# Kernel tuning notes

Measured on AMD Instinct MI355X. Metric: run time of the kernel, lower is better.

The kernel has to match this reference:

```python
import jax, jax.numpy as jnp
import numpy as np

INPUT_DIM = 1024
HIDDEN_DIM = 1024

def setup_inputs() -> dict:
    key = jax.random.key(0)
    ks = jax.random.split(key, 9)
    s_in = 1.0 / np.sqrt(INPUT_DIM)
    s_h = 1.0 / np.sqrt(HIDDEN_DIM)
    x = jax.random.normal(ks[0], (4, 2048, INPUT_DIM), dtype=jnp.float32)
    Wq = jax.random.uniform(ks[1], (INPUT_DIM, HIDDEN_DIM), jnp.float32, -s_in, s_in)
    bq = jax.random.uniform(ks[2], (HIDDEN_DIM,), jnp.float32, -s_in, s_in)
    Wk = jax.random.uniform(ks[3], (INPUT_DIM, HIDDEN_DIM), jnp.float32, -s_in, s_in)
    bk = jax.random.uniform(ks[4], (HIDDEN_DIM,), jnp.float32, -s_in, s_in)
    Wv = jax.random.uniform(ks[5], (INPUT_DIM, HIDDEN_DIM), jnp.float32, -s_in, s_in)
    bv = jax.random.uniform(ks[6], (HIDDEN_DIM,), jnp.float32, -s_in, s_in)
    Wo = jax.random.uniform(ks[7], (HIDDEN_DIM, INPUT_DIM), jnp.float32, -s_h, s_h)
    bo = jax.random.uniform(ks[8], (INPUT_DIM,), jnp.float32, -s_h, s_h)
    return {"x": x, "Wq": Wq, "bq": bq, "Wk": Wk, "bk": bk, "Wv": Wv, "bv": bv, "Wo": Wo, "bo": bo}

def reference(x, Wq, bq, Wk, bk, Wv, bv, Wo, bo):
    # x: [B, S, D_in]; scale uses x.shape[-1] (faithful to source, which divides by sqrt(input_dim))
    scale = 1.0 / jnp.sqrt(jnp.asarray(x.shape[-1], dtype=x.dtype))
    Q = jnp.einsum('bsd,dh->bsh', x, Wq) + bq
    K = jnp.einsum('bsd,dh->bsh', x, Wk) + bk
    V = jnp.einsum('bsd,dh->bsh', x, Wv) + bv
    scores = jnp.einsum('bqh,bkh->bqk', Q, K) * scale  # [B, S, S]
    attn = jax.nn.softmax(scores, axis=-1)
    ctx = jnp.einsum('bqk,bkh->bqh', attn, V)
    return jnp.einsum('bsh,hd->bsd', ctx, Wo) + bo
```

## Files before the change

### kernel.cpp

```cpp
#include <hip/hip_runtime.h>
#include <hip/hip_bf16.h>

typedef __attribute__((ext_vector_type(8))) short bf16x8;
typedef __attribute__((ext_vector_type(16))) float f32x16;
typedef __attribute__((ext_vector_type(4))) unsigned short us4;

#define AS1 __attribute__((address_space(1)))
#define AS3 __attribute__((address_space(3)))

__device__ __forceinline__ unsigned short f2bf(float f) {
  unsigned u = __float_as_uint(f);
  u += 0x7fff + ((u >> 16) & 1);
  return (unsigned short)(u >> 16);
}

__device__ __forceinline__ float bf2f(unsigned short h) {
  return __uint_as_float((unsigned)h << 16);
}

__device__ __forceinline__ void gload_lds16(const void* g, void* l) {
  __builtin_amdgcn_global_load_lds((const AS1 unsigned int*)g,
                                   (AS3 unsigned int*)l, 16, 0, 0);
}

template <typename OutT, bool BIAS, int MODE, int NJ>
__global__ __launch_bounds__(256, (NJ >= 3) ? 2 : 3) void gemm_bt(
    const unsigned short* __restrict__ A,
    const unsigned short* __restrict__ Bt,
    OutT* __restrict__ C,
    unsigned short* __restrict__ Vt,
    const float* __restrict__ bias,
    int Kd, int lda, int ldb, int ldc,
    long sA, long sB, long sC,
    float scale) {
  constexpr int BN    = NJ * 64;
  constexpr int ROWS  = 128 + BN;
  constexpr int SLOTS = ROWS / 16;
  __shared__ unsigned short lds[2][ROWS * 32];

  const int bz = blockIdx.z;
  A  += (size_t)bz * sA + (size_t)blockIdx.x * 128 * lda;
  Bt += (size_t)bz * sB + (size_t)blockIdx.y * BN * ldb;

  const int tid  = threadIdx.x;
  const int wave = tid >> 6;
  const int lane = tid & 63;
  const int wm   = (wave >> 1) * 64;
  const int wn   = (wave & 1) * (NJ * 32);
  const int l32  = lane & 31;
  const int half = lane >> 5;
  const int cg   = ((lane & 3) ^ ((lane >> 2) & 3) ^ (lane >> 4)) * 8;
  const int pswz = (l32 & 3) ^ ((l32 >> 2) & 3);

  auto stage = [&](int k0, int b) {
#pragma unroll
    for (int j = 0; j < SLOTS / 4; ++j) {
      const int s = wave + 4 * j;
      const int r = s * 16 + (lane >> 2);
      const unsigned short* src = (s < 8) ? (A + (size_t)r * lda)
                                          : (Bt + (size_t)(r - 128) * ldb);
      gload_lds16(src + k0 + cg, (char*)&lds[b][0] + s * 1024);
    }
  };

  f32x16 acc[2][NJ] = {};

  stage(0, 0);
  int cur = 0;
  for (int k0 = 0; k0 < Kd; k0 += 32) {
    __syncthreads();
    if (k0 + 32 < Kd) stage(k0 + 32, cur ^ 1);

    const unsigned short* base = &lds[cur][0];
    bf16x8 af[2][2], bfr[NJ][2];
#pragma unroll
    for (int t = 0; t < 2; ++t)
#pragma unroll
      for (int h = 0; h < 2; ++h) {
        const int p = ((2 * h + half) ^ pswz) * 8;
        af[t][h] = *(const bf16x8*)&base[(wm + t * 32 + l32) * 32 + p];
      }
#pragma unroll
    for (int u = 0; u < NJ; ++u)
#pragma unroll
      for (int h = 0; h < 2; ++h) {
        const int p = ((2 * h + half) ^ pswz) * 8;
        bfr[u][h] = *(const bf16x8*)&base[(128 + wn + u * 32 + l32) * 32 + p];
      }
#pragma unroll
    for (int t = 0; t < 2; ++t)
#pragma unroll
      for (int u = 0; u < NJ; ++u) {
        acc[t][u] = __builtin_amdgcn_mfma_f32_32x32x16_bf16(af[t][0], bfr[u][0], acc[t][u], 0, 0, 0);
        acc[t][u] = __builtin_amdgcn_mfma_f32_32x32x16_bf16(af[t][1], bfr[u][1], acc[t][u], 0, 0, 0);
      }
    cur ^= 1;
  }

  const int row0 = blockIdx.x * 128 + wm;
  const int colb = blockIdx.y * BN;

  if constexpr (MODE == 1) {
#pragma unroll
    for (int t = 0; t < 2; ++t) {
#pragma unroll
      for (int u = 0; u < NJ; ++u) {
        const int gcol  = colb + wn + u * 32;
        const int piece = gcol >> 10;
        const float bv  = BIAS ? bias[gcol + l32] : 0.0f;
        if (piece < 2) {
          OutT* dst = C + (size_t)piece * sC;
          const int col = (gcol & 1023) + l32;
#pragma unroll
          for (int r = 0; r < 16; ++r) {
            const int row = row0 + t * 32 + (r & 3) + 8 * (r >> 2) + 4 * half;
            dst[(size_t)row * ldc + col] = (OutT)f2bf(acc[t][u][r] * scale + bv);
          }
        } else {
          const int d = (gcol & 1023) + l32;
          const int b = row0 >> 11;
          const int sbase = (row0 & 2047) + t * 32 + 4 * half;
#pragma unroll
          for (int g = 0; g < 4; ++g) {
            const int s0 = sbase + 8 * g;
            us4 pk;
            pk.x = f2bf(acc[t][u][4 * g + 0] * scale + bv);
            pk.y = f2bf(acc[t][u][4 * g + 1] * scale + bv);
            pk.z = f2bf(acc[t][u][4 * g + 2] * scale + bv);
            pk.w = f2bf(acc[t][u][4 * g + 3] * scale + bv);
            *(us4*)&Vt[((size_t)b << 21) + (size_t)d * 2048 + s0] = pk;
          }
        }
      }
    }
  } else {
    C += (size_t)bz * sC;
    const int col0 = colb + wn;
#pragma unroll
    for (int t = 0; t < 2; ++t) {
#pragma unroll
      for (int u = 0; u < NJ; ++u) {
        const int col = col0 + u * 32 + l32;
        const float bv = BIAS ? bias[col0 + u * 32 + l32] : 0.0f;
#pragma unroll
        for (int r = 0; r < 16; ++r) {
          const int row = row0 + t * 32 + (r & 3) + 8 * (r >> 2) + 4 * half;
          const float v = acc[t][u][r] * scale + bv;
          if constexpr (sizeof(OutT) == 4)
            C[(size_t)row * ldc + col] = v;
          else
            C[(size_t)row * ldc + col] = (OutT)f2bf(v);
        }
      }
    }
  }
}

__global__ void cvt_x(const float* __restrict__ in, unsigned short* __restrict__ out, int n4) {
  const int i = blockIdx.x * blockDim.x + threadIdx.x;
  if (i < n4) {
    const float4 v = ((const float4*)in)[i];
    uint2 o;
    o.x = (unsigned)f2bf(v.x) | ((unsigned)f2bf(v.y) << 16);
    o.y = (unsigned)f2bf(v.z) | ((unsigned)f2bf(v.w) << 16);
    ((uint2*)out)[i] = o;
  }
}

__global__ void cvtT_w4(const float* __restrict__ Wq, const float* __restrict__ Wk,
                        const float* __restrict__ Wv, const float* __restrict__ Wo,
                        unsigned short* __restrict__ Wqkvb, unsigned short* __restrict__ Wob) {
  __shared__ unsigned short tile[64][65];
  const int z = blockIdx.z;
  const float* in = (z == 0) ? Wq : (z == 1) ? Wk : (z == 2) ? Wv : Wo;
  unsigned short* out = (z == 3) ? Wob : Wqkvb + (size_t)z * 1024 * 1024;
  const int r0 = blockIdx.y * 64, c0 = blockIdx.x * 64;
  for (int i = threadIdx.y; i < 64; i += 4)
    tile[i][threadIdx.x] = f2bf(in[(size_t)(r0 + i) * 1024 + c0 + threadIdx.x]);
  __syncthreads();
  for (int i = threadIdx.y; i < 64; i += 4)
    out[(size_t)(c0 + i) * 1024 + r0 + threadIdx.x] = tile[threadIdx.x][i];
}

__global__ void concat_bias(const float* __restrict__ bq, const float* __restrict__ bk,
                            const float* __restrict__ bv, float* __restrict__ dst) {
  const int z = blockIdx.x;
  const float* src = (z == 0) ? bq : (z == 1) ? bk : bv;
  const int i = threadIdx.x;
  ((float4*)(dst + z * 1024))[i] = ((const float4*)src)[i];
}

__global__ __launch_bounds__(256) void softmax_bf16(unsigned short* __restrict__ scores) {
  unsigned short* p = scores + (size_t)blockIdx.x * 2048;
  const int t = threadIdx.x;
  uint4 raw = ((const uint4*)p)[t];
  float v[8];
  v[0] = __uint_as_float(raw.x << 16); v[1] = __uint_as_float(raw.x & 0xffff0000u);
  v[2] = __uint_as_float(raw.y << 16); v[3] = __uint_as_float(raw.y & 0xffff0000u);
  v[4] = __uint_as_float(raw.z << 16); v[5] = __uint_as_float(raw.z & 0xffff0000u);
  v[6] = __uint_as_float(raw.w << 16); v[7] = __uint_as_float(raw.w & 0xffff0000u);

  float m = v[0];
#pragma unroll
  for (int i = 1; i < 8; ++i) m = fmaxf(m, v[i]);
#pragma unroll
  for (int off = 32; off; off >>= 1) m = fmaxf(m, __shfl_xor(m, off, 64));

  __shared__ float red[4];
  __shared__ float bcast[2];
  const int wave = t >> 6, lane = t & 63;
  if (lane == 0) red[wave] = m;
  __syncthreads();
  if (t == 0) bcast[0] = fmaxf(fmaxf(red[0], red[1]), fmaxf(red[2], red[3]));
  __syncthreads();
  m = bcast[0];

  float s = 0.f;
#pragma unroll
  for (int i = 0; i < 8; ++i) { v[i] = __expf(v[i] - m); s += v[i]; }
#pragma unroll
  for (int off = 32; off; off >>= 1) s += __shfl_xor(s, off, 64);
  if (lane == 0) red[wave] = s;
  __syncthreads();
  if (t == 0) bcast[1] = red[0] + red[1] + red[2] + red[3];
  __syncthreads();
  const float inv = 1.0f / bcast[1];

  uint4 ov;
  ov.x = (unsigned)f2bf(v[0] * inv) | ((unsigned)f2bf(v[1] * inv) << 16);
  ov.y = (unsigned)f2bf(v[2] * inv) | ((unsigned)f2bf(v[3] * inv) << 16);
  ov.z = (unsigned)f2bf(v[4] * inv) | ((unsigned)f2bf(v[5] * inv) << 16);
  ov.w = (unsigned)f2bf(v[6] * inv) | ((unsigned)f2bf(v[7] * inv) << 16);
  ((uint4*)p)[t] = ov;
}

extern "C" void kernel_launch(void* const* d_in, const int* in_sizes, int n_in,
                              void* d_out, int out_size, void* d_ws, size_t ws_size,
                              hipStream_t stream) {
  const float* x  = (const float*)d_in[0];
  const float* Wq = (const float*)d_in[1];
  const float* bq = (const float*)d_in[2];
  const float* Wk = (const float*)d_in[3];
  const float* bk = (const float*)d_in[4];
  const float* Wv = (const float*)d_in[5];
  const float* bv = (const float*)d_in[6];
  const float* Wo = (const float*)d_in[7];
  const float* bo = (const float*)d_in[8];
  float* out = (float*)d_out;

  char* ws = (char*)d_ws;
  size_t off = 0;
  auto alloc = [&](size_t bytes) { char* p = ws + off; off += (bytes + 255) & ~255UL; return p; };
  unsigned short* xb    = (unsigned short*)alloc(8192UL * 1024 * 2);
  unsigned short* Wqkvb = (unsigned short*)alloc(3072UL * 1024 * 2);
  unsigned short* Wob   = (unsigned short*)alloc(1024UL * 1024 * 2);
  float*          bqkv  = (float*)alloc(3072UL * 4);
  unsigned short* Qb    = (unsigned short*)alloc(8192UL * 1024 * 2);
  unsigned short* Kb    = (unsigned short*)alloc(8192UL * 1024 * 2);
  unsigned short* Vtb   = (unsigned short*)alloc(4UL * 1024 * 2048 * 2);
  unsigned short* attn  = (unsigned short*)alloc(8192UL * 2048 * 2);
  unsigned short* ctxb  = (unsigned short*)alloc(8192UL * 1024 * 2);

  const dim3 blk(256);

  cvt_x<<<2097152 / 256, 256, 0, stream>>>(x, xb, 2097152);
  cvtT_w4<<<dim3(16, 16, 4), dim3(64, 4), 0, stream>>>(Wq, Wk, Wv, Wo, Wqkvb, Wob);
  concat_bias<<<3, 256, 0, stream>>>(bq, bk, bv, bqkv);

  gemm_bt<unsigned short, true, 1, 3><<<dim3(64, 16, 1), blk, 0, stream>>>(
      xb, Wqkvb, Qb, Vtb, bqkv, 1024, 1024, 1024, 1024, 0, 0, 8192L * 1024, 1.0f);

  gemm_bt<unsigned short, false, 0, 4><<<dim3(16, 8, 4), blk, 0, stream>>>(
      Qb, Kb, attn, nullptr, nullptr, 1024, 1024, 1024, 2048,
      2048L * 1024, 2048L * 1024, 2048L * 2048, 0.03125f);

  softmax_bf16<<<8192, 256, 0, stream>>>(attn);

  gemm_bt<unsigned short, false, 0, 2><<<dim3(16, 8, 4), blk, 0, stream>>>(
      attn, Vtb, ctxb, nullptr, nullptr, 2048, 2048, 2048, 1024,
      2048L * 2048, 1024L * 2048, 2048L * 1024, 1.0f);

  gemm_bt<float, true, 0, 2><<<dim3(64, 8, 1), blk, 0, stream>>>(
      ctxb, Wob, out, nullptr, bo, 1024, 1024, 1024, 1024, 0, 0, 0, 1.0f);
}
```

Before: 300.2 us.

## Load B operand directly from global into registers, bypassing LDS

The B tile is no longer staged through shared memory. Each wave now loads its B fragments straight from global memory into registers with double buffering, and only A goes through LDS. The main loop is unrolled by two with fixed buffer indices. This is meant to shrink LDS use and LDS read traffic, and the launch bounds are set to 2 blocks for every NJ. In exchange, global loads are no longer shared across waves: waves with the same wn load the same B data redundantly. Register pressure also rises, and occupancy may drop for small NJ.

```diff
diff --git a/kernel.cpp b/kernel.cpp
--- a/kernel.cpp
+++ b/kernel.cpp
@@ -14,17 +14,13 @@
   return (unsigned short)(u >> 16);
 }
 
-__device__ __forceinline__ float bf2f(unsigned short h) {
-  return __uint_as_float((unsigned)h << 16);
-}
-
 __device__ __forceinline__ void gload_lds16(const void* g, void* l) {
   __builtin_amdgcn_global_load_lds((const AS1 unsigned int*)g,
                                    (AS3 unsigned int*)l, 16, 0, 0);
 }
 
 template <typename OutT, bool BIAS, int MODE, int NJ>
-__global__ __launch_bounds__(256, (NJ >= 3) ? 2 : 3) void gemm_bt(
+__global__ __launch_bounds__(256, 2) void gemm_bt(
     const unsigned short* __restrict__ A,
     const unsigned short* __restrict__ Bt,
     OutT* __restrict__ C,
@@ -33,10 +29,8 @@
     int Kd, int lda, int ldb, int ldc,
     long sA, long sB, long sC,
     float scale) {
-  constexpr int BN    = NJ * 64;
-  constexpr int ROWS  = 128 + BN;
-  constexpr int SLOTS = ROWS / 16;
-  __shared__ unsigned short lds[2][ROWS * 32];
+  constexpr int BN = NJ * 64;
+  __shared__ unsigned short lds[2][128 * 32];
 
   const int bz = blockIdx.z;
   A  += (size_t)bz * sA + (size_t)blockIdx.x * 128 * lda;
@@ -52,27 +46,29 @@
   const int cg   = ((lane & 3) ^ ((lane >> 2) & 3) ^ (lane >> 4)) * 8;
   const int pswz = (l32 & 3) ^ ((l32 >> 2) & 3);
 
-  auto stage = [&](int k0, int b) {
-#pragma unroll
-    for (int j = 0; j < SLOTS / 4; ++j) {
+  const unsigned short* Bp = Bt + (size_t)(wn + l32) * ldb + 8 * half;
+
+  auto stageA = [&](int k0, int b) {
+#pragma unroll
+    for (int j = 0; j < 2; ++j) {
       const int s = wave + 4 * j;
       const int r = s * 16 + (lane >> 2);
-      const unsigned short* src = (s < 8) ? (A + (size_t)r * lda)
-                                          : (Bt + (size_t)(r - 128) * ldb);
-      gload_lds16(src + k0 + cg, (char*)&lds[b][0] + s * 1024);
+      gload_lds16(A + (size_t)r * lda + k0 + cg, (char*)&lds[b][0] + s * 1024);
     }
   };
+  auto loadB = [&](int k0, bf16x8 (&b)[NJ][2]) {
+#pragma unroll
+    for (int u = 0; u < NJ; ++u)
+#pragma unroll
+      for (int h = 0; h < 2; ++h)
+        b[u][h] = *(const bf16x8*)(Bp + (size_t)u * 32 * ldb + k0 + 16 * h);
+  };
 
   f32x16 acc[2][NJ] = {};
 
-  stage(0, 0);
-  int cur = 0;
-  for (int k0 = 0; k0 < Kd; k0 += 32) {
-    __syncthreads();
-    if (k0 + 32 < Kd) stage(k0 + 32, cur ^ 1);
-
-    const unsigned short* base = &lds[cur][0];
-    bf16x8 af[2][2], bfr[NJ][2];
+  auto compute = [&](int b, bf16x8 (&bf)[NJ][2]) {
+    const unsigned short* base = &lds[b][0];
+    bf16x8 af[2][2];
 #pragma unroll
     for (int t = 0; t < 2; ++t)
 #pragma unroll
@@ -81,20 +77,24 @@
         af[t][h] = *(const bf16x8*)&base[(wm + t * 32 + l32) * 32 + p];
       }
 #pragma unroll
-    for (int u = 0; u < NJ; ++u)
-#pragma unroll
-      for (int h = 0; h < 2; ++h) {
-        const int p = ((2 * h + half) ^ pswz) * 8;
-        bfr[u][h] = *(const bf16x8*)&base[(128 + wn + u * 32 + l32) * 32 + p];
-      }
-#pragma unroll
     for (int t = 0; t < 2; ++t)
 #pragma unroll
       for (int u = 0; u < NJ; ++u) {
-        acc[t][u] = __builtin_amdgcn_mfma_f32_32x32x16_bf16(af[t][0], bfr[u][0], acc[t][u], 0, 0, 0);
-        acc[t][u] = __builtin_amdgcn_mfma_f32_32x32x16_bf16(af[t][1], bfr[u][1], acc[t][u], 0, 0, 0);
-      }
-    cur ^= 1;
+        acc[t][u] = __builtin_amdgcn_mfma_f32_32x32x16_bf16(af[t][0], bf[u][0], acc[t][u], 0, 0, 0);
+        acc[t][u] = __builtin_amdgcn_mfma_f32_32x32x16_bf16(af[t][1], bf[u][1], acc[t][u], 0, 0, 0);
+      }
+  };
+
+  bf16x8 b0[NJ][2], b1[NJ][2];
+  stageA(0, 0);
+  loadB(0, b0);
+  for (int k0 = 0; k0 < Kd; k0 += 64) {
+    __syncthreads();
+    if (k0 + 32 < Kd) { stageA(k0 + 32, 1); loadB(k0 + 32, b1); }
+    compute(0, b0);
+    __syncthreads();
+    if (k0 + 64 < Kd) { stageA(k0 + 64, 0); loadB(k0 + 64, b0); }
+    compute(1, b1);
   }
 
   const int row0 = blockIdx.x * 128 + wm;
```

New measurement: 416.2 us. 1.39x slower.
